# Optimization experiments

Measured on AMD Instinct MI355X. Metric: run time of the kernel, lower is better.

Reference implementation:

```python
import jax, jax.numpy as jnp
import numpy as np


def setup_inputs() -> dict:
    key = jax.random.key(0)
    k1, k2, k3 = jax.random.split(key, 3)
    B, C_in, C_out, T = 16, 512, 512, 4096
    pre = jax.random.normal(k1, (B, C_in, T), dtype=jnp.float32)
    # nn.Linear weight layout: [out_features, in_features]
    W_pre = jax.random.normal(k2, (C_out, C_in), dtype=jnp.float32) * (1.0 / np.sqrt(C_in))
    b_pre = jax.random.normal(k3, (C_out,), dtype=jnp.float32) * 0.01
    return {"pre": pre, "W_pre": W_pre, "b_pre": b_pre}


def reference(pre, W_pre, b_pre):
    # Original 'casual' branch loops over T applying w_pre(_pre[:,:,i]) into BOTH
    # embedding_prev and embedding_curr, then sums -> 2 * (W_pre @ pre + b).
    # Batched form: one einsum over the full sequence.
    y = jnp.einsum('bct,oc->bot', pre, W_pre) + b_pre[None, :, None]  # [B, C_out, T]
    return y + y
```

## Files before the change

kernel.cpp:

```cpp
#include <hip/hip_runtime.h>
#include <hip/hip_bf16.h>

typedef __attribute__((ext_vector_type(8))) short short8_t;
typedef __attribute__((ext_vector_type(4))) float f32x4;

#define BATCH 16
#define CIN   512
#define COUT  512
#define TT    4096
#define BKT   32
#define NKT   16

__device__ __forceinline__ uint pk2(float a, float b) {
    ushort lo = __builtin_bit_cast(ushort, __float2bfloat16(a));
    ushort hi = __builtin_bit_cast(ushort, __float2bfloat16(b));
    return (uint)lo | ((uint)hi << 16);
}

#define SCHEDB()   __builtin_amdgcn_sched_barrier(0)
#define WAIT_VM(N) do { asm volatile("s_waitcnt vmcnt(" #N ")" ::: "memory"); SCHEDB(); } while (0)
#define WAIT_LGKM() do { asm volatile("s_waitcnt lgkmcnt(0)" ::: "memory"); SCHEDB(); } while (0)
#define RAW_BARRIER() do { __builtin_amdgcn_s_barrier(); SCHEDB(); } while (0)

extern "C" __global__ __launch_bounds__(256)
void wconv(const float* __restrict__ W, ushort* __restrict__ Wb)
{
    const int i  = blockIdx.x * 256 + threadIdx.x;
    const int m  = i >> 7;
    const int k0 = (i & 127) * 4;
    const float4 v = *(const float4*)(W + (size_t)m * CIN + k0);
    const int bm = m >> 4, r = m & 15;
    const int ksg = k0 >> 5, g = (k0 >> 3) & 3, k7 = k0 & 7;
    uint2 q;
    q.x = pk2(v.x, v.y);
    q.y = pk2(v.z, v.w);
    *(uint2*)&Wb[(size_t)bm * 8192 + ksg * 512 + g * 128 + r * 8 + k7] = q;
}

template<bool WSB>
__global__ __launch_bounds__(256)
void conv2x1_gemm(const float* __restrict__ pre, const float* __restrict__ W,
                  const ushort* __restrict__ Wb,
                  const float* __restrict__ bias, float* __restrict__ out)
{
    __shared__ float  RAW[3][BKT * 64];
    __shared__ ushort BF [2][4 * 64 * 8];

    const int tid  = threadIdx.x;
    const int lane = tid & 63;
    const int wv   = tid >> 6;
    const int g    = lane >> 4;
    const int l15  = lane & 15;

    const int id   = ((blockIdx.x & 7) << 8) | (blockIdx.x >> 3);
    const int mblk = id & 1;
    const int ti   = (id >> 1) & 63;
    const int bb   = id >> 7;

    const int m0 = mblk << 8;
    const int t0 = ti << 6;

    const float* preB   = pre + (size_t)bb * ((size_t)CIN * TT);
    const int    bmBase = (m0 >> 4) + wv * 4;

    f32x4 acc[4][4];
#pragma unroll
    for (int i = 0; i < 4; ++i)
#pragma unroll
        for (int j = 0; j < 4; ++j) acc[i][j] = (f32x4)0.0f;

    short8_t afA[4], afB[4];

#define STAGE(J) do { \
    _Pragma("unroll") \
    for (int i = 0; i < 2; ++i) { \
        const int krow = wv*8 + i*4 + (lane >> 4); \
        const float* gsrc = preB + (size_t)((J)*BKT + krow) * TT + t0 + ((lane & 15) << 2); \
        float* ldst = &RAW[(J) % 3][(wv*128 + i*64 + lane) * 4]; \
        __builtin_amdgcn_global_load_lds((const __attribute__((address_space(1))) void*)gsrc, \
                                         (__attribute__((address_space(3))) void*)ldst, 16, 0, 0); \
    } } while (0)

#define LOAD_A(KT, AF) do { \
    if constexpr (WSB) { \
        _Pragma("unroll") \
        for (int mi = 0; mi < 4; ++mi) \
            AF[mi] = *(const short8_t*)(Wb + (size_t)(bmBase + mi) * 8192 \
                                        + (KT) * 512 + g * 128 + l15 * 8); \
    } else { \
        _Pragma("unroll") \
        for (int mi = 0; mi < 4; ++mi) { \
            const float* ab = W + (size_t)(m0 + wv*64 + mi*16 + l15) * CIN + (KT)*BKT + g*8; \
            const float4 u0 = *(const float4*)ab; \
            const float4 u1 = *(const float4*)(ab + 4); \
            uint4 qq; \
            qq.x = pk2(u0.x, u0.y); qq.y = pk2(u0.z, u0.w); \
            qq.z = pk2(u1.x, u1.y); qq.w = pk2(u1.z, u1.w); \
            AF[mi] = __builtin_bit_cast(short8_t, qq); \
        } \
    } } while (0)

#define CVT(J) do { \
    const int ct = tid & 63; \
    float f[8]; \
    _Pragma("unroll") \
    for (int j = 0; j < 8; ++j) \
        f[j] = RAW[(J) % 3][(wv*8 + j) * 64 + ct]; \
    uint4 q; \
    q.x = pk2(f[0], f[1]); \
    q.y = pk2(f[2], f[3]); \
    q.z = pk2(f[4], f[5]); \
    q.w = pk2(f[6], f[7]); \
    *(uint4*)&BF[(J) & 1][wv * 512 + ct * 8] = q; \
    } while (0)

#define MFMA_STEP(J, AF) do { \
    short8_t bf[4]; \
    _Pragma("unroll") \
    for (int ni = 0; ni < 4; ++ni) \
        bf[ni] = *(const short8_t*)&BF[(J) & 1][g * 512 + (ni*16 + l15) * 8]; \
    _Pragma("unroll") \
    for (int mi = 0; mi < 4; ++mi) \
        _Pragma("unroll") \
        for (int ni = 0; ni < 4; ++ni) \
            acc[mi][ni] = __builtin_amdgcn_mfma_f32_16x16x32_bf16(AF[mi], bf[ni], acc[mi][ni], 0, 0, 0); \
    } while (0)

    STAGE(0);
    STAGE(1);
    LOAD_A(0, afA);
    WAIT_VM(6);
    RAW_BARRIER();
    CVT(0);

#pragma unroll
    for (int kt = 0; kt < NKT; ++kt) {
        if (kt + 1 < NKT) {
            if ((kt & 1) == 0) LOAD_A(kt + 1, afB);
            else               LOAD_A(kt + 1, afA);
        }
        if (kt + 2 < NKT) STAGE(kt + 2);
        if      (kt + 2 < NKT) WAIT_VM(6);
        else if (kt + 1 < NKT) WAIT_VM(4);
        else                   WAIT_VM(0);
        WAIT_LGKM();
        RAW_BARRIER();
        if ((kt & 1) == 0) MFMA_STEP(kt, afA);
        else               MFMA_STEP(kt, afB);
        if (kt + 1 < NKT) CVT(kt + 1);
    }

    const int orow = m0 + wv*64 + g*4;
    float bv[4][4];
#pragma unroll
    for (int mi = 0; mi < 4; ++mi)
#pragma unroll
        for (int r = 0; r < 4; ++r)
            bv[mi][r] = bias[orow + mi*16 + r];

    float* outB = out + (size_t)bb * ((size_t)COUT * TT);
#pragma unroll
    for (int mi = 0; mi < 4; ++mi) {
#pragma unroll
        for (int ni = 0; ni < 4; ++ni) {
            const int t = t0 + ni*16 + l15;
#pragma unroll
            for (int r = 0; r < 4; ++r) {
                const int o = orow + mi*16 + r;
                outB[(size_t)o * TT + t] = 2.0f * (acc[mi][ni][r] + bv[mi][r]);
            }
        }
    }
}

extern "C" void kernel_launch(void* const* d_in, const int* in_sizes, int n_in,
                              void* d_out, int out_size, void* d_ws, size_t ws_size,
                              hipStream_t stream)
{
    const float* pre  = (const float*)d_in[0];
    const float* Wp   = (const float*)d_in[1];
    const float* bias = (const float*)d_in[2];
    float* out = (float*)d_out;

    const size_t wb_bytes = (size_t)COUT * CIN * sizeof(ushort);

    const dim3 grid(BATCH * 2 * 64);
    const dim3 block(256);

    if (ws_size >= wb_bytes) {
        ushort* Wb = (ushort*)d_ws;
        hipLaunchKernelGGL(wconv, dim3(256), dim3(256), 0, stream, Wp, Wb);
        hipLaunchKernelGGL((conv2x1_gemm<true>), grid, block, 0, stream,
                           pre, Wp, Wb, bias, out);
    } else {
        hipLaunchKernelGGL((conv2x1_gemm<false>), grid, block, 0, stream,
                           pre, Wp, (const ushort*)nullptr, bias, out);
    }
}
```

Before: 72.28 us.

## Double the K tile to 64 and split the convert into read/write around the MFMAs

Raises the K tile from 32 to 64, which halves the number of main-loop iterations and barriers. Each iteration now issues twice as many staged loads and A-fragment loads, and the vmcnt wait counts are adjusted to match. The fp32-to-bf16 conversion is split so the LDS reads are issued before the MFMA block and the bf16 writes after it, letting LDS latency overlap with matrix math. MFMA priority is raised with setprio. The cost is more registers and LDS per block, which may reduce occupancy.

Result: slower. 75.90 us (+5.0%).

```diff
diff --git a/kernel.cpp b/kernel.cpp
--- a/kernel.cpp
+++ b/kernel.cpp
@@ -8,8 +8,8 @@
 #define CIN   512
 #define COUT  512
 #define TT    4096
-#define BKT   32
-#define NKT   16
+#define BKT   64
+#define NKT   8
 
 __device__ __forceinline__ uint pk2(float a, float b) {
     ushort lo = __builtin_bit_cast(ushort, __float2bfloat16(a));
@@ -44,7 +44,7 @@
                   const float* __restrict__ bias, float* __restrict__ out)
 {
     __shared__ float  RAW[3][BKT * 64];
-    __shared__ ushort BF [2][4 * 64 * 8];
+    __shared__ ushort BF [2][8 * 64 * 8];
 
     const int tid  = threadIdx.x;
     const int lane = tid & 63;
@@ -62,6 +62,7 @@
 
     const float* preB   = pre + (size_t)bb * ((size_t)CIN * TT);
     const int    bmBase = (m0 >> 4) + wv * 4;
+    const int    ct     = tid & 63;
 
     f32x4 acc[4][4];
 #pragma unroll
@@ -69,14 +70,15 @@
 #pragma unroll
         for (int j = 0; j < 4; ++j) acc[i][j] = (f32x4)0.0f;
 
-    short8_t afA[4], afB[4];
+    short8_t afA[2][4], afB[2][4];
+    float    f[16];
 
 #define STAGE(J) do { \
     _Pragma("unroll") \
-    for (int i = 0; i < 2; ++i) { \
-        const int krow = wv*8 + i*4 + (lane >> 4); \
+    for (int i = 0; i < 4; ++i) { \
+        const int krow = wv*16 + i*4 + (lane >> 4); \
         const float* gsrc = preB + (size_t)((J)*BKT + krow) * TT + t0 + ((lane & 15) << 2); \
-        float* ldst = &RAW[(J) % 3][(wv*128 + i*64 + lane) * 4]; \
+        float* ldst = &RAW[(J) % 3][(wv*16 + i*4)*64 + lane*4]; \
         __builtin_amdgcn_global_load_lds((const __attribute__((address_space(1))) void*)gsrc, \
                                          (__attribute__((address_space(3))) void*)ldst, 16, 0, 0); \
     } } while (0)
@@ -84,54 +86,68 @@
 #define LOAD_A(KT, AF) do { \
     if constexpr (WSB) { \
         _Pragma("unroll") \
+        for (int ks = 0; ks < 2; ++ks) \
+            _Pragma("unroll") \
+            for (int mi = 0; mi < 4; ++mi) \
+                AF[ks][mi] = *(const short8_t*)(Wb + (size_t)(bmBase + mi) * 8192 \
+                                                + ((KT)*2 + ks) * 512 + g * 128 + l15 * 8); \
+    } else { \
+        _Pragma("unroll") \
+        for (int ks = 0; ks < 2; ++ks) \
+            _Pragma("unroll") \
+            for (int mi = 0; mi < 4; ++mi) { \
+                const float* ab = W + (size_t)(m0 + wv*64 + mi*16 + l15) * CIN \
+                                  + (KT)*BKT + ks*32 + g*8; \
+                const float4 u0 = *(const float4*)ab; \
+                const float4 u1 = *(const float4*)(ab + 4); \
+                uint4 qq; \
+                qq.x = pk2(u0.x, u0.y); qq.y = pk2(u0.z, u0.w); \
+                qq.z = pk2(u1.x, u1.y); qq.w = pk2(u1.z, u1.w); \
+                AF[ks][mi] = __builtin_bit_cast(short8_t, qq); \
+            } \
+    } } while (0)
+
+#define CVT_READ(J) do { \
+    _Pragma("unroll") \
+    for (int j = 0; j < 16; ++j) \
+        f[j] = RAW[(J) % 3][(wv*16 + j) * 64 + ct]; \
+    } while (0)
+
+#define CVT_WRITE(J) do { \
+    _Pragma("unroll") \
+    for (int h = 0; h < 2; ++h) { \
+        uint4 q; \
+        q.x = pk2(f[h*8+0], f[h*8+1]); \
+        q.y = pk2(f[h*8+2], f[h*8+3]); \
+        q.z = pk2(f[h*8+4], f[h*8+5]); \
+        q.w = pk2(f[h*8+6], f[h*8+7]); \
+        *(uint4*)&BF[(J) & 1][(wv*2 + h) * 512 + ct * 8] = q; \
+    } } while (0)
+
+#define MFMA_STEP(J, AF) do { \
+    __builtin_amdgcn_s_setprio(1); \
+    _Pragma("unroll") \
+    for (int ks = 0; ks < 2; ++ks) { \
+        short8_t bf[4]; \
+        _Pragma("unroll") \
+        for (int ni = 0; ni < 4; ++ni) \
+            bf[ni] = *(const short8_t*)&BF[(J) & 1][(ks*4 + g) * 512 + (ni*16 + l15) * 8]; \
+        _Pragma("unroll") \
         for (int mi = 0; mi < 4; ++mi) \
-            AF[mi] = *(const short8_t*)(Wb + (size_t)(bmBase + mi) * 8192 \
-                                        + (KT) * 512 + g * 128 + l15 * 8); \
-    } else { \
-        _Pragma("unroll") \
-        for (int mi = 0; mi < 4; ++mi) { \
-            const float* ab = W + (size_t)(m0 + wv*64 + mi*16 + l15) * CIN + (KT)*BKT + g*8; \
-            const float4 u0 = *(const float4*)ab; \
-            const float4 u1 = *(const float4*)(ab + 4); \
-            uint4 qq; \
-            qq.x = pk2(u0.x, u0.y); qq.y = pk2(u0.z, u0.w); \
-            qq.z = pk2(u1.x, u1.y); qq.w = pk2(u1.z, u1.w); \
-            AF[mi] = __builtin_bit_cast(short8_t, qq); \
-        } \
-    } } while (0)
-
-#define CVT(J) do { \
-    const int ct = tid & 63; \
-    float f[8]; \
-    _Pragma("unroll") \
-    for (int j = 0; j < 8; ++j) \
-        f[j] = RAW[(J) % 3][(wv*8 + j) * 64 + ct]; \
-    uint4 q; \
-    q.x = pk2(f[0], f[1]); \
-    q.y = pk2(f[2], f[3]); \
-    q.z = pk2(f[4], f[5]); \
-    q.w = pk2(f[6], f[7]); \
-    *(uint4*)&BF[(J) & 1][wv * 512 + ct * 8] = q; \
-    } while (0)
-
-#define MFMA_STEP(J, AF) do { \
-    short8_t bf[4]; \
-    _Pragma("unroll") \
-    for (int ni = 0; ni < 4; ++ni) \
-        bf[ni] = *(const short8_t*)&BF[(J) & 1][g * 512 + (ni*16 + l15) * 8]; \
-    _Pragma("unroll") \
-    for (int mi = 0; mi < 4; ++mi) \
-        _Pragma("unroll") \
-        for (int ni = 0; ni < 4; ++ni) \
-            acc[mi][ni] = __builtin_amdgcn_mfma_f32_16x16x32_bf16(AF[mi], bf[ni], acc[mi][ni], 0, 0, 0); \
+            _Pragma("unroll") \
+            for (int ni = 0; ni < 4; ++ni) \
+                acc[mi][ni] = __builtin_amdgcn_mfma_f32_16x16x32_bf16(AF[ks][mi], bf[ni], acc[mi][ni], 0, 0, 0); \
+    } \
+    __builtin_amdgcn_s_setprio(0); \
     } while (0)
 
     STAGE(0);
     STAGE(1);
     LOAD_A(0, afA);
-    WAIT_VM(6);
+    WAIT_VM(12);
     RAW_BARRIER();
-    CVT(0);
+    CVT_READ(0);
+    CVT_WRITE(0);
 
 #pragma unroll
     for (int kt = 0; kt < NKT; ++kt) {
@@ -140,14 +156,15 @@
             else               LOAD_A(kt + 1, afA);
         }
         if (kt + 2 < NKT) STAGE(kt + 2);
-        if      (kt + 2 < NKT) WAIT_VM(6);
-        else if (kt + 1 < NKT) WAIT_VM(4);
+        if      (kt + 2 < NKT) WAIT_VM(12);
+        else if (kt + 1 < NKT) WAIT_VM(8);
         else                   WAIT_VM(0);
         WAIT_LGKM();
         RAW_BARRIER();
+        if (kt + 1 < NKT) CVT_READ(kt + 1);
         if ((kt & 1) == 0) MFMA_STEP(kt, afA);
         else               MFMA_STEP(kt, afB);
-        if (kt + 1 < NKT) CVT(kt + 1);
+        if (kt + 1 < NKT) CVT_WRITE(kt + 1);
     }
 
     const int orow = m0 + wv*64 + g*4;
```

## Deepen activation prefetch to three stages and overlap LDS reads with MFMA

Applied to the files above, without the earlier changes.

Grows the raw LDS ring from three to four buffers so global-to-LDS loads of activations run three k-tiles ahead, with the vmcnt waits retuned to match. The fp32-to-bf16 conversion is split so its LDS reads are issued before the MFMA block and the packing and stores after it, hiding LDS latency behind the matrix math. MFMA sections also raise wave priority via s_setprio. The cost is more LDS per block, which may reduce occupancy, and more live registers held across the MFMA block.

Measured after the change: 74.77 us, median of 2. 1.03x slower.

```diff
diff --git a/kernel.cpp b/kernel.cpp
--- a/kernel.cpp
+++ b/kernel.cpp
@@ -17,8 +17,11 @@
     return (uint)lo | ((uint)hi << 16);
 }
 
-#define SCHEDB()   __builtin_amdgcn_sched_barrier(0)
-#define WAIT_VM(N) do { asm volatile("s_waitcnt vmcnt(" #N ")" ::: "memory"); SCHEDB(); } while (0)
+#define SCHEDB()    __builtin_amdgcn_sched_barrier(0)
+#define WAIT_VM0()  do { asm volatile("s_waitcnt vmcnt(0)" ::: "memory"); SCHEDB(); } while (0)
+#define WAIT_VM4()  do { asm volatile("s_waitcnt vmcnt(4)" ::: "memory"); SCHEDB(); } while (0)
+#define WAIT_VM6()  do { asm volatile("s_waitcnt vmcnt(6)" ::: "memory"); SCHEDB(); } while (0)
+#define WAIT_VM8()  do { asm volatile("s_waitcnt vmcnt(8)" ::: "memory"); SCHEDB(); } while (0)
 #define WAIT_LGKM() do { asm volatile("s_waitcnt lgkmcnt(0)" ::: "memory"); SCHEDB(); } while (0)
 #define RAW_BARRIER() do { __builtin_amdgcn_s_barrier(); SCHEDB(); } while (0)
 
@@ -43,7 +46,7 @@
                   const ushort* __restrict__ Wb,
                   const float* __restrict__ bias, float* __restrict__ out)
 {
-    __shared__ float  RAW[3][BKT * 64];
+    __shared__ float  RAW[4][BKT * 64];
     __shared__ ushort BF [2][4 * 64 * 8];
 
     const int tid  = threadIdx.x;
@@ -70,13 +73,14 @@
         for (int j = 0; j < 4; ++j) acc[i][j] = (f32x4)0.0f;
 
     short8_t afA[4], afB[4];
+    float    f[8];
 
 #define STAGE(J) do { \
     _Pragma("unroll") \
     for (int i = 0; i < 2; ++i) { \
         const int krow = wv*8 + i*4 + (lane >> 4); \
         const float* gsrc = preB + (size_t)((J)*BKT + krow) * TT + t0 + ((lane & 15) << 2); \
-        float* ldst = &RAW[(J) % 3][(wv*128 + i*64 + lane) * 4]; \
+        float* ldst = &RAW[(J) % 4][(wv*128 + i*64 + lane) * 4]; \
         __builtin_amdgcn_global_load_lds((const __attribute__((address_space(1))) void*)gsrc, \
                                          (__attribute__((address_space(3))) void*)ldst, 16, 0, 0); \
     } } while (0)
@@ -100,12 +104,15 @@
         } \
     } } while (0)
 
-#define CVT(J) do { \
+#define CVT_READ(J) do { \
     const int ct = tid & 63; \
-    float f[8]; \
     _Pragma("unroll") \
     for (int j = 0; j < 8; ++j) \
-        f[j] = RAW[(J) % 3][(wv*8 + j) * 64 + ct]; \
+        f[j] = RAW[(J) % 4][(wv*8 + j) * 64 + ct]; \
+    } while (0)
+
+#define CVT_WRITE(J) do { \
+    const int ct = tid & 63; \
     uint4 q; \
     q.x = pk2(f[0], f[1]); \
     q.y = pk2(f[2], f[3]); \
@@ -115,6 +122,7 @@
     } while (0)
 
 #define MFMA_STEP(J, AF) do { \
+    __builtin_amdgcn_s_setprio(1); \
     short8_t bf[4]; \
     _Pragma("unroll") \
     for (int ni = 0; ni < 4; ++ni) \
@@ -124,14 +132,17 @@
         _Pragma("unroll") \
         for (int ni = 0; ni < 4; ++ni) \
             acc[mi][ni] = __builtin_amdgcn_mfma_f32_16x16x32_bf16(AF[mi], bf[ni], acc[mi][ni], 0, 0, 0); \
+    __builtin_amdgcn_s_setprio(0); \
     } while (0)
 
     STAGE(0);
     STAGE(1);
+    STAGE(2);
     LOAD_A(0, afA);
-    WAIT_VM(6);
+    WAIT_VM8();
     RAW_BARRIER();
-    CVT(0);
+    CVT_READ(0);
+    CVT_WRITE(0);
 
 #pragma unroll
     for (int kt = 0; kt < NKT; ++kt) {
@@ -139,15 +150,18 @@
             if ((kt & 1) == 0) LOAD_A(kt + 1, afB);
             else               LOAD_A(kt + 1, afA);
         }
-        if (kt + 2 < NKT) STAGE(kt + 2);
-        if      (kt + 2 < NKT) WAIT_VM(6);
-        else if (kt + 1 < NKT) WAIT_VM(4);
-        else                   WAIT_VM(0);
+        if (kt + 3 < NKT) STAGE(kt + 3);
+        if      (kt == 0)  WAIT_VM6();
+        else if (kt <= 12) WAIT_VM8();
+        else if (kt == 13) WAIT_VM6();
+        else if (kt == 14) WAIT_VM4();
+        else               WAIT_VM0();
         WAIT_LGKM();
         RAW_BARRIER();
+        if (kt + 1 < NKT) CVT_READ(kt + 1);
         if ((kt & 1) == 0) MFMA_STEP(kt, afA);
         else               MFMA_STEP(kt, afB);
-        if (kt + 1 < NKT) CVT(kt + 1);
+        if (kt + 1 < NKT) CVT_WRITE(kt + 1);
     }
 
     const int orow = m0 + wv*64 + g*4;
```
